# Optimization experiments

Hardware: AMD Instinct MI355X
Metric: run time of the kernel (lower is better)

The kernel has to match this reference:

```python
import jax, jax.numpy as jnp
import numpy as np

NSAMPLES = [64, 32, 16, 8, 4]
TEMPERATURE = 1.0


def square_distance(src, dst):
    # src [B,N,C], dst [B,M,C] -> [B,N,M]
    d = -2.0 * jnp.einsum('bnc,bmc->bnm', src, dst)
    d = d + jnp.sum(src ** 2, -1)[:, :, None]
    d = d + jnp.sum(dst ** 2, -1)[:, None, :]
    return d


def knn_point(nsample, xyz, new_xyz):
    # indices of nsample nearest points in xyz for each query in new_xyz
    sqrdists = square_distance(new_xyz, xyz)           # [B,S,N]
    _, idx = jax.lax.top_k(-sqrdists, nsample)         # smallest distances
    return idx                                         # [B,S,nsample]


def index_points(points, idx):
    # points [B,N,C], idx [B,S,K] -> [B,S,K,C]
    B, S, K = idx.shape
    flat = idx.reshape(B, S * K)
    out = jnp.take_along_axis(points, flat[..., None], axis=1)
    return out.reshape(B, S, K, points.shape[-1])


def boundary_loss(labels, coords, feats, num_classes):
    onehot = jax.nn.one_hot(labels, num_classes, dtype=jnp.float32)  # [B,N,C]
    loss = jnp.float32(0.0)
    for i, (coord, feat) in enumerate(zip(coords, feats)):
        if i == 0:
            probability_labels = onehot
        else:
            kneighbors = i * 4
            nb_idx = knn_point(kneighbors, coords[0], coord)          # [B,Ni,k]
            probability_labels = index_points(onehot, nb_idx).mean(-2)  # [B,Ni,C]
        nsample = NSAMPLES[i]
        neighbor_indexs = knn_point(nsample, coord, coord)            # [B,Ni,ns]
        neighbor_labels = index_points(probability_labels, neighbor_indexs)  # [B,Ni,ns,C]
        neighbor_feats = index_points(feat, neighbor_indexs)          # [B,Ni,ns,D]
        center_label = jnp.argmax(probability_labels, -1)[:, :, None]  # [B,Ni,1]
        neighbor_label = jnp.argmax(neighbor_labels, -1)               # [B,Ni,ns]
        mask = (center_label == neighbor_label)                        # [B,Ni,ns] bool
        cnt = jnp.sum(mask.astype(jnp.int32), -1)
        point_mask = (cnt > 0) & (cnt < nsample)                       # [B,Ni]
        any_pm = jnp.any(point_mask)
        pm = point_mask.astype(jnp.float32)[:, :, None]                # [B,Ni,1]
        # pairwise feature distances to the nsample neighbors
        diff = feat[:, :, None, :] - neighbor_feats                    # [B,Ni,ns,D]
        dist = jnp.sqrt(jnp.sum(diff ** 2, -1) + 1e-6)                 # [B,Ni,ns]
        dist = -dist
        dist = dist - jnp.max(dist, -1, keepdims=True)
        dist = dist / TEMPERATURE
        exp = jnp.exp(dist)
        pos = jnp.sum(exp * mask.astype(jnp.float32) * pm)
        neg = jnp.sum(exp * pm)
        pos = jnp.where(any_pm, pos, 1.0)
        neg = jnp.where(any_pm, neg, 1.0)
        term = -jnp.log(pos / (neg + 1e-6))
        loss = loss + jnp.where(any_pm, term, 0.0)
    return loss


def setup_inputs() -> dict:
    key = jax.random.key(0)
    ks = jax.random.split(key, 12)
    B, N = 2, 4096
    sizes = [N, N // 4, N // 16, N // 64, N // 256]
    inp = {}
    inp['labels'] = jax.random.randint(ks[0], (B, N), 0, 21)
    for i, s in enumerate(sizes):
        inp[f'coord{i}'] = jax.random.normal(ks[1 + i], (B, s, 3), dtype=jnp.float32)
        inp[f'feat{i}'] = jax.random.normal(ks[6 + i], (B, s, 32), dtype=jnp.float32)
    inp['num_classes'] = 21
    return inp


def reference(labels, coord0, coord1, coord2, coord3, coord4,
              feat0, feat1, feat2, feat3, feat4, num_classes):
    coords = [coord0, coord1, coord2, coord3, coord4]
    feats = [feat0, feat1, feat2, feat3, feat4]
    return boundary_loss(labels, coords, feats, num_classes)
```

## Files before the change

kernel.cpp:

```cpp
#include <hip/hip_runtime.h>
#include <math.h>

#define WAVE 64
#define NC 21

__device__ __forceinline__ unsigned f32_ord(float f) {
    unsigned u = __float_as_uint(f);
    return (u & 0x80000000u) ? ~u : (u | 0x80000000u);
}

__device__ __forceinline__ unsigned wave_min_u32(unsigned v) {
#pragma unroll
    for (int off = 32; off >= 1; off >>= 1) {
        unsigned o = (unsigned)__shfl_xor((int)v, off, WAVE);
        v = (o < v) ? o : v;
    }
    return v;
}

__device__ __forceinline__ float wave_max_f32(float v) {
#pragma unroll
    for (int off = 32; off >= 1; off >>= 1)
        v = fmaxf(v, __shfl_xor(v, off, WAVE));
    return v;
}

__device__ __forceinline__ float wave_sum_f32(float v) {
#pragma unroll
    for (int off = 32; off >= 1; off >>= 1)
        v += __shfl_xor(v, off, WAVE);
    return v;
}

struct SelShm {
    int hist[4][256];
    int sel[64];
    int swave[4];
    int scnt;
};

__device__ __forceinline__ void radix_scan_step(SelShm& shm, int lane,
                                                int& need, unsigned& Vhi) {
    int i0 = 4 * lane;
    int b0 = shm.hist[0][i0]   + shm.hist[1][i0]   + shm.hist[2][i0]   + shm.hist[3][i0];
    int b1 = shm.hist[0][i0+1] + shm.hist[1][i0+1] + shm.hist[2][i0+1] + shm.hist[3][i0+1];
    int b2 = shm.hist[0][i0+2] + shm.hist[1][i0+2] + shm.hist[2][i0+2] + shm.hist[3][i0+2];
    int b3 = shm.hist[0][i0+3] + shm.hist[1][i0+3] + shm.hist[2][i0+3] + shm.hist[3][i0+3];
    int lsum = b0 + b1 + b2 + b3;
    int c = lsum;
#pragma unroll
    for (int off = 1; off < 64; off <<= 1) {
        int o = __shfl_up(c, off, WAVE);
        c += (lane >= off) ? o : 0;
    }
    unsigned long long mball = __ballot(c >= need);
    int Ls = __ffsll((unsigned long long)mball) - 1;
    int cL = __shfl(c, Ls, WAVE);
    int lsumL = __shfl(lsum, Ls, WAVE);
    int B0 = __shfl(b0, Ls, WAVE);
    int B1 = __shfl(b1, Ls, WAVE);
    int B2 = __shfl(b2, Ls, WAVE);
    int e = cL - lsumL;
    int T;
    if (e + B0 >= need)                { T = 4 * Ls + 0; }
    else if (e + B0 + B1 >= need)      { T = 4 * Ls + 1; e += B0; }
    else if (e + B0 + B1 + B2 >= need) { T = 4 * Ls + 2; e += B0 + B1; }
    else                               { T = 4 * Ls + 3; e += B0 + B1 + B2; }
    need -= e;
    Vhi = (Vhi << 8) | (unsigned)T;
}

template <int NI, int NS>
__device__ __forceinline__ void block_select_topNS(
    const float* __restrict__ rp,
    float qx, float qy, float qz, float nq,
    SelShm& shm, int tid)
{
    constexpr int NPL = (NI + 255) / 256;
    constexpr bool FULL = (NPL * 256 == NI);
    const int lane = tid & 63;
    const int wid = tid >> 6;
    const unsigned long long lmask = (1ull << lane) - 1ull;

    unsigned ok[NPL];
#pragma unroll
    for (int j = 0; j < NPL; ++j) {
        int g = j * 256 + tid;
        unsigned o = 0xFFFFFFFFu;
        if (FULL || g < NI) {
            float rx = rp[3*g], ry = rp[3*g+1], rz = rp[3*g+2];
            float nr = rx*rx + ry*ry + rz*rz;
            float dot = qx*rx + qy*ry + qz*rz;
            o = f32_ord(-2.0f*dot + nq + nr);
        }
        ok[j] = o;
    }

    int* hf = &shm.hist[0][0];
#pragma unroll
    for (int i = 0; i < 4; ++i) hf[i * 256 + tid] = 0;
    if (tid == 0) shm.scnt = 0;
    __syncthreads();

    int need = NS;
    unsigned Vhi = 0;

#pragma unroll
    for (int j = 0; j < NPL; ++j)
        atomicAdd(&shm.hist[wid][ok[j] >> 24], 1);
    __syncthreads();
    radix_scan_step(shm, lane, need, Vhi);
    __syncthreads();
#pragma unroll
    for (int i = 0; i < 4; ++i) hf[i * 256 + tid] = 0;
    __syncthreads();

#pragma unroll
    for (int pass = 1; pass < 4; ++pass) {
        const int shift = 24 - 8 * pass;
#pragma unroll
        for (int j = 0; j < NPL; ++j) {
            if ((ok[j] >> (shift + 8)) == Vhi)
                atomicAdd(&shm.hist[wid][(ok[j] >> shift) & 255], 1);
        }
        __syncthreads();
        radix_scan_step(shm, lane, need, Vhi);
        __syncthreads();
        if (pass < 3) {
#pragma unroll
            for (int i = 0; i < 4; ++i) hf[i * 256 + tid] = 0;
            __syncthreads();
        }
    }

    const unsigned V = Vhi;
    const int R = need;
    const int clt = NS - R;

#pragma unroll
    for (int j = 0; j < NPL; ++j) {
        bool s = ok[j] < V;
        unsigned long long mk = __ballot(s);
        int n = __popcll(mk);
        if (n) {
            int wb = 0;
            if (lane == 0) wb = atomicAdd(&shm.scnt, n);
            wb = __shfl(wb, 0, WAVE);
            if (s) shm.sel[wb + __popcll(mk & lmask)] = j * 256 + tid;
        }
    }

    unsigned consumed = 0u;
    for (int r = 0; r < R; ++r) {
        int bj = -1;
#pragma unroll
        for (int j = NPL - 1; j >= 0; --j)
            if (ok[j] == V && !((consumed >> j) & 1u)) bj = j;
        unsigned g = (bj >= 0) ? (unsigned)(bj * 256 + tid) : 0xFFFFFFFFu;
        unsigned mg = wave_min_u32(g);
        if (lane == 0) shm.swave[wid] = (int)mg;
        __syncthreads();
        unsigned t0 = (unsigned)shm.swave[0], t1 = (unsigned)shm.swave[1];
        unsigned t2 = (unsigned)shm.swave[2], t3 = (unsigned)shm.swave[3];
        unsigned ta = (t0 < t1) ? t0 : t1;
        unsigned tb = (t2 < t3) ? t2 : t3;
        unsigned t = (ta < tb) ? ta : tb;
        if (bj >= 0 && g == t) consumed |= (1u << bj);
        if (tid == 0) shm.sel[clt + r] = (int)t;
        __syncthreads();
    }
}

template <int NQ, int K>
__device__ __forceinline__ void knn_level(
    const float* __restrict__ qc, const float* __restrict__ rc,
    const int* __restrict__ rl, int* __restrict__ out,
    int qb, SelShm& shm, int tid)
{
    int b = qb / NQ, qi = qb - b * NQ;
    const float* qp = qc + ((long)b * NQ + qi) * 3;
    float qx = qp[0], qy = qp[1], qz = qp[2];
    float nq = qx*qx + qy*qy + qz*qz;
    block_select_topNS<4096, K>(rc + (long)b * 4096 * 3, qx, qy, qz, nq, shm, tid);
    if ((tid >> 6) == 0) {
        int lane = tid & 63;
        int lb = (lane < K) ? rl[(long)b * 4096 + shm.sel[lane]] : -1;
        int cnt = 0;
#pragma unroll
        for (int k = 0; k < K; ++k) {
            int lk = __shfl(lb, k, WAVE);
            cnt += (lk == lane) ? 1 : 0;
        }
        int key = (lane < NC) ? ((cnt << 8) | (255 - lane)) : 0;
#pragma unroll
        for (int off = 32; off >= 1; off >>= 1) {
            int o = __shfl_xor(key, off, WAVE);
            key = (o > key) ? o : key;
        }
        if (lane == 0) out[(long)b * NQ + qi] = 255 - (key & 255);
    }
}

template <int NI, int NS>
__device__ __forceinline__ void boundary_level(
    const float* __restrict__ coord, const float* __restrict__ feat,
    const int* __restrict__ lbl,
    double* __restrict__ pos, double* __restrict__ neg, int* __restrict__ anyf,
    int qb, SelShm& shm, int tid)
{
    int b = qb / NI, qi = qb - b * NI;
    const float* qp = coord + ((long)b * NI + qi) * 3;
    float qx = qp[0], qy = qp[1], qz = qp[2];
    float nq = qx*qx + qy*qy + qz*qz;
    block_select_topNS<NI, NS>(coord + (long)b * NI * 3, qx, qy, qz, nq, shm, tid);
    if ((tid >> 6) == 0) {
        int lane = tid & 63;
        int center = lbl[(long)b * NI + qi];
        bool m = false;
        float dj = -INFINITY;
        if (lane < NS) {
            int nb = shm.sel[lane];
            m = (lbl[(long)b * NI + nb] == center);
            const float4* fq = (const float4*)(feat + ((long)b * NI + qi) * 32);
            const float4* fn = (const float4*)(feat + ((long)b * NI + nb) * 32);
            float s = 0.f;
#pragma unroll
            for (int d = 0; d < 8; ++d) {
                float4 a = fq[d], c = fn[d];
                float d0 = a.x - c.x, d1 = a.y - c.y;
                float d2 = a.z - c.z, d3 = a.w - c.w;
                s += d0*d0 + d1*d1 + d2*d2 + d3*d3;
            }
            dj = -sqrtf(s + 1e-6f);
        }
        unsigned long long mb = __ballot(m);
        int cnt = __popcll(mb);
        float mxv = wave_max_f32(dj);
        float ej = 0.f, pj = 0.f;
        if (lane < NS) {
            ej = expf(dj - mxv);
            pj = m ? ej : 0.f;
        }
        float se = wave_sum_f32(ej);
        float sp = wave_sum_f32(pj);
        bool pm = (cnt > 0) && (cnt < NS);
        if (pm && lane == 0) {
            atomicAdd(pos, (double)sp);
            atomicAdd(neg, (double)se);
            *anyf = 1;
        }
    }
}

__global__ __launch_bounds__(256) void knn_fused(
    const float* __restrict__ c1, const float* __restrict__ c2,
    const float* __restrict__ c3, const float* __restrict__ c4,
    const float* __restrict__ c0, const int* __restrict__ labels,
    int* __restrict__ lbl1, int* __restrict__ lbl2,
    int* __restrict__ lbl3, int* __restrict__ lbl4,
    double* __restrict__ posA, double* __restrict__ negA,
    int* __restrict__ anyA, int B)
{
    __shared__ SelShm shm;
    int blk = blockIdx.x, tid = threadIdx.x;
    int n1 = B * 1024, n2 = n1 + B * 256, n3 = n2 + B * 64, n4 = n3 + B * 16;
    if (blk < n1)      knn_level<1024, 4>(c1, c0, labels, lbl1, blk,      shm, tid);
    else if (blk < n2) knn_level<256,  8>(c2, c0, labels, lbl2, blk - n1, shm, tid);
    else if (blk < n3) knn_level<64,  12>(c3, c0, labels, lbl3, blk - n2, shm, tid);
    else if (blk < n4) knn_level<16,  16>(c4, c0, labels, lbl4, blk - n3, shm, tid);
    else if (tid < 5) { posA[tid] = 0.0; negA[tid] = 0.0; anyA[tid] = 0; }
}

__global__ __launch_bounds__(256) void boundary_fused(
    const float* __restrict__ c0, const float* __restrict__ c1,
    const float* __restrict__ c2, const float* __restrict__ c3,
    const float* __restrict__ c4,
    const float* __restrict__ f0, const float* __restrict__ f1,
    const float* __restrict__ f2, const float* __restrict__ f3,
    const float* __restrict__ f4,
    const int* __restrict__ labels, const int* __restrict__ lbl1,
    const int* __restrict__ lbl2, const int* __restrict__ lbl3,
    const int* __restrict__ lbl4,
    double* __restrict__ posA, double* __restrict__ negA,
    int* __restrict__ anyA, int B)
{
    __shared__ SelShm shm;
    int blk = blockIdx.x, tid = threadIdx.x;
    int m0 = B * 4096, m1 = m0 + B * 1024, m2 = m1 + B * 256;
    int m3 = m2 + B * 64, m4 = m3 + B * 16;
    if (blk < m0)
        boundary_level<4096, 64>(c0, f0, labels, posA+0, negA+0, anyA+0, blk,      shm, tid);
    else if (blk < m1)
        boundary_level<1024, 32>(c1, f1, lbl1,   posA+1, negA+1, anyA+1, blk - m0, shm, tid);
    else if (blk < m2)
        boundary_level<256,  16>(c2, f2, lbl2,   posA+2, negA+2, anyA+2, blk - m1, shm, tid);
    else if (blk < m3)
        boundary_level<64,    8>(c3, f3, lbl3,   posA+3, negA+3, anyA+3, blk - m2, shm, tid);
    else if (blk < m4)
        boundary_level<16,    4>(c4, f4, lbl4,   posA+4, negA+4, anyA+4, blk - m3, shm, tid);
}

__global__ void finalize_kernel(const double* __restrict__ pos,
                                const double* __restrict__ neg,
                                const int* __restrict__ anyf,
                                float* __restrict__ out) {
    if (threadIdx.x == 0 && blockIdx.x == 0) {
        float loss = 0.f;
        for (int i = 0; i < 5; ++i) {
            if (anyf[i]) {
                float p = (float)pos[i];
                float n = (float)neg[i];
                loss += -logf(p / (n + 1e-6f));
            }
        }
        out[0] = loss;
    }
}

extern "C" void kernel_launch(void* const* d_in, const int* in_sizes, int n_in,
                              void* d_out, int out_size, void* d_ws, size_t ws_size,
                              hipStream_t stream) {
    (void)out_size; (void)ws_size;
    const int* labels = (const int*)d_in[0];
    const float* coord[5];
    const float* feat[5];
    bool interleaved = (n_in >= 3 && in_sizes[2] == 2 * 4096 * 32);
    if (interleaved) {
        for (int i = 0; i < 5; ++i) {
            coord[i] = (const float*)d_in[1 + 2 * i];
            feat[i]  = (const float*)d_in[2 + 2 * i];
        }
    } else {
        for (int i = 0; i < 5; ++i) {
            coord[i] = (const float*)d_in[1 + i];
            feat[i]  = (const float*)d_in[6 + i];
        }
    }
    int B = in_sizes[0] / 4096;

    double* posA = (double*)d_ws;
    double* negA = posA + 5;
    int* anyA = (int*)(negA + 5);
    int* lbl1 = anyA + 8;
    int* lbl2 = lbl1 + B * 1024;
    int* lbl3 = lbl2 + B * 256;
    int* lbl4 = lbl3 + B * 64;

    int knn_grid = B * (1024 + 256 + 64 + 16) + 1;
    hipLaunchKernelGGL(knn_fused, dim3(knn_grid), dim3(256), 0, stream,
                       coord[1], coord[2], coord[3], coord[4],
                       coord[0], labels, lbl1, lbl2, lbl3, lbl4,
                       posA, negA, anyA, B);

    int bnd_grid = B * (4096 + 1024 + 256 + 64 + 16);
    hipLaunchKernelGGL(boundary_fused, dim3(bnd_grid), dim3(256), 0, stream,
                       coord[0], coord[1], coord[2], coord[3], coord[4],
                       feat[0], feat[1], feat[2], feat[3], feat[4],
                       labels, lbl1, lbl2, lbl3, lbl4,
                       posA, negA, anyA, B);

    hipLaunchKernelGGL(finalize_kernel, dim3(1), dim3(1), 0, stream,
                       posA, negA, anyA, (float*)d_out);
}
```

Measured before the change: 448.8 us.

## Replace block radix-select kNN with per-wave bitonic top-k with threshold skipping

Swaps the per-query 256-thread block radix select (shared-memory histograms, many __syncthreads, serial tie resolution) for one wavefront per query. Each wave keeps a sorted top-64 list in registers via a bitonic sort and, chunk by chunk, merges in new candidates only when some lane beats the current k-th threshold. This drops the shared memory and block barriers and packs four queries per block. The trade-off is that each wave now scans all reference points itself, so cost depends on how often chunks pass the threshold. Ties are broken by index through the packed 64-bit keys.

Result: slower. 614.9 us (+37.0%).

```diff
diff --git a/kernel.cpp b/kernel.cpp
--- a/kernel.cpp
+++ b/kernel.cpp
@@ -9,15 +9,6 @@
     return (u & 0x80000000u) ? ~u : (u | 0x80000000u);
 }
 
-__device__ __forceinline__ unsigned wave_min_u32(unsigned v) {
-#pragma unroll
-    for (int off = 32; off >= 1; off >>= 1) {
-        unsigned o = (unsigned)__shfl_xor((int)v, off, WAVE);
-        v = (o < v) ? o : v;
-    }
-    return v;
-}
-
 __device__ __forceinline__ float wave_max_f32(float v) {
 #pragma unroll
     for (int off = 32; off >= 1; off >>= 1)
@@ -32,173 +23,104 @@
     return v;
 }
 
-struct SelShm {
-    int hist[4][256];
-    int sel[64];
-    int swave[4];
-    int scnt;
-};
-
-__device__ __forceinline__ void radix_scan_step(SelShm& shm, int lane,
-                                                int& need, unsigned& Vhi) {
-    int i0 = 4 * lane;
-    int b0 = shm.hist[0][i0]   + shm.hist[1][i0]   + shm.hist[2][i0]   + shm.hist[3][i0];
-    int b1 = shm.hist[0][i0+1] + shm.hist[1][i0+1] + shm.hist[2][i0+1] + shm.hist[3][i0+1];
-    int b2 = shm.hist[0][i0+2] + shm.hist[1][i0+2] + shm.hist[2][i0+2] + shm.hist[3][i0+2];
-    int b3 = shm.hist[0][i0+3] + shm.hist[1][i0+3] + shm.hist[2][i0+3] + shm.hist[3][i0+3];
-    int lsum = b0 + b1 + b2 + b3;
-    int c = lsum;
-#pragma unroll
-    for (int off = 1; off < 64; off <<= 1) {
-        int o = __shfl_up(c, off, WAVE);
-        c += (lane >= off) ? o : 0;
-    }
-    unsigned long long mball = __ballot(c >= need);
-    int Ls = __ffsll((unsigned long long)mball) - 1;
-    int cL = __shfl(c, Ls, WAVE);
-    int lsumL = __shfl(lsum, Ls, WAVE);
-    int B0 = __shfl(b0, Ls, WAVE);
-    int B1 = __shfl(b1, Ls, WAVE);
-    int B2 = __shfl(b2, Ls, WAVE);
-    int e = cL - lsumL;
-    int T;
-    if (e + B0 >= need)                { T = 4 * Ls + 0; }
-    else if (e + B0 + B1 >= need)      { T = 4 * Ls + 1; e += B0; }
-    else if (e + B0 + B1 + B2 >= need) { T = 4 * Ls + 2; e += B0 + B1; }
-    else                               { T = 4 * Ls + 3; e += B0 + B1 + B2; }
-    need -= e;
-    Vhi = (Vhi << 8) | (unsigned)T;
+__device__ __forceinline__ unsigned long long bitonic_sort64(
+    unsigned long long v, int lane)
+{
+#pragma unroll
+    for (int k = 2; k <= 64; k <<= 1) {
+#pragma unroll
+        for (int j = k >> 1; j > 0; j >>= 1) {
+            unsigned long long o = __shfl_xor(v, j, WAVE);
+            bool take_min = (((lane & j) == 0) == ((lane & k) == 0));
+            unsigned long long mn = (v < o) ? v : o;
+            unsigned long long mx = (v < o) ? o : v;
+            v = take_min ? mn : mx;
+        }
+    }
+    return v;
+}
+
+__device__ __forceinline__ unsigned long long bitonic_merge_keep_low(
+    unsigned long long h, unsigned long long c, int lane)
+{
+    unsigned long long cr = __shfl(c, 63 - lane, WAVE);
+    unsigned long long v = (h < cr) ? h : cr;
+#pragma unroll
+    for (int j = 32; j > 0; j >>= 1) {
+        unsigned long long o = __shfl_xor(v, j, WAVE);
+        bool take_min = ((lane & j) == 0);
+        unsigned long long mn = (v < o) ? v : o;
+        unsigned long long mx = (v < o) ? o : v;
+        v = take_min ? mn : mx;
+    }
+    return v;
 }
 
 template <int NI, int NS>
-__device__ __forceinline__ void block_select_topNS(
+__device__ __forceinline__ unsigned long long wave_topk(
     const float* __restrict__ rp,
-    float qx, float qy, float qz, float nq,
-    SelShm& shm, int tid)
-{
-    constexpr int NPL = (NI + 255) / 256;
-    constexpr bool FULL = (NPL * 256 == NI);
-    const int lane = tid & 63;
-    const int wid = tid >> 6;
-    const unsigned long long lmask = (1ull << lane) - 1ull;
-
-    unsigned ok[NPL];
-#pragma unroll
-    for (int j = 0; j < NPL; ++j) {
-        int g = j * 256 + tid;
-        unsigned o = 0xFFFFFFFFu;
-        if (FULL || g < NI) {
+    float qx, float qy, float qz, float nq, int lane)
+{
+    constexpr int NCH = (NI + 63) / 64;
+
+    unsigned long long h;
+    {
+        unsigned long long p = ~0ull;
+        if (NI >= 64 || lane < NI) {
+            int g = lane;
             float rx = rp[3*g], ry = rp[3*g+1], rz = rp[3*g+2];
             float nr = rx*rx + ry*ry + rz*rz;
             float dot = qx*rx + qy*ry + qz*rz;
-            o = f32_ord(-2.0f*dot + nq + nr);
-        }
-        ok[j] = o;
-    }
-
-    int* hf = &shm.hist[0][0];
-#pragma unroll
-    for (int i = 0; i < 4; ++i) hf[i * 256 + tid] = 0;
-    if (tid == 0) shm.scnt = 0;
-    __syncthreads();
-
-    int need = NS;
-    unsigned Vhi = 0;
-
-#pragma unroll
-    for (int j = 0; j < NPL; ++j)
-        atomicAdd(&shm.hist[wid][ok[j] >> 24], 1);
-    __syncthreads();
-    radix_scan_step(shm, lane, need, Vhi);
-    __syncthreads();
-#pragma unroll
-    for (int i = 0; i < 4; ++i) hf[i * 256 + tid] = 0;
-    __syncthreads();
-
-#pragma unroll
-    for (int pass = 1; pass < 4; ++pass) {
-        const int shift = 24 - 8 * pass;
-#pragma unroll
-        for (int j = 0; j < NPL; ++j) {
-            if ((ok[j] >> (shift + 8)) == Vhi)
-                atomicAdd(&shm.hist[wid][(ok[j] >> shift) & 255], 1);
-        }
-        __syncthreads();
-        radix_scan_step(shm, lane, need, Vhi);
-        __syncthreads();
-        if (pass < 3) {
-#pragma unroll
-            for (int i = 0; i < 4; ++i) hf[i * 256 + tid] = 0;
-            __syncthreads();
-        }
-    }
-
-    const unsigned V = Vhi;
-    const int R = need;
-    const int clt = NS - R;
-
-#pragma unroll
-    for (int j = 0; j < NPL; ++j) {
-        bool s = ok[j] < V;
-        unsigned long long mk = __ballot(s);
-        int n = __popcll(mk);
-        if (n) {
-            int wb = 0;
-            if (lane == 0) wb = atomicAdd(&shm.scnt, n);
-            wb = __shfl(wb, 0, WAVE);
-            if (s) shm.sel[wb + __popcll(mk & lmask)] = j * 256 + tid;
-        }
-    }
-
-    unsigned consumed = 0u;
-    for (int r = 0; r < R; ++r) {
-        int bj = -1;
-#pragma unroll
-        for (int j = NPL - 1; j >= 0; --j)
-            if (ok[j] == V && !((consumed >> j) & 1u)) bj = j;
-        unsigned g = (bj >= 0) ? (unsigned)(bj * 256 + tid) : 0xFFFFFFFFu;
-        unsigned mg = wave_min_u32(g);
-        if (lane == 0) shm.swave[wid] = (int)mg;
-        __syncthreads();
-        unsigned t0 = (unsigned)shm.swave[0], t1 = (unsigned)shm.swave[1];
-        unsigned t2 = (unsigned)shm.swave[2], t3 = (unsigned)shm.swave[3];
-        unsigned ta = (t0 < t1) ? t0 : t1;
-        unsigned tb = (t2 < t3) ? t2 : t3;
-        unsigned t = (ta < tb) ? ta : tb;
-        if (bj >= 0 && g == t) consumed |= (1u << bj);
-        if (tid == 0) shm.sel[clt + r] = (int)t;
-        __syncthreads();
-    }
+            unsigned o = f32_ord(-2.0f*dot + nq + nr);
+            p = ((unsigned long long)o << 32) | (unsigned)g;
+        }
+        h = bitonic_sort64(p, lane);
+    }
+    if (NCH > 1) {
+        unsigned long long tau = __shfl(h, NS - 1, WAVE);
+#pragma unroll 1
+        for (int cch = 1; cch < NCH; ++cch) {
+            int g = cch * 64 + lane;
+            float rx = rp[3*g], ry = rp[3*g+1], rz = rp[3*g+2];
+            float nr = rx*rx + ry*ry + rz*rz;
+            float dot = qx*rx + qy*ry + qz*rz;
+            unsigned o = f32_ord(-2.0f*dot + nq + nr);
+            unsigned long long p = ((unsigned long long)o << 32) | (unsigned)g;
+            if (__ballot(p < tau) == 0ull) continue;
+            unsigned long long cs = bitonic_sort64(p, lane);
+            h = bitonic_merge_keep_low(h, cs, lane);
+            tau = __shfl(h, NS - 1, WAVE);
+        }
+    }
+    return h;
 }
 
 template <int NQ, int K>
 __device__ __forceinline__ void knn_level(
     const float* __restrict__ qc, const float* __restrict__ rc,
-    const int* __restrict__ rl, int* __restrict__ out,
-    int qb, SelShm& shm, int tid)
-{
-    int b = qb / NQ, qi = qb - b * NQ;
+    const int* __restrict__ rl, int* __restrict__ out, int q, int lane)
+{
+    int b = q / NQ, qi = q - b * NQ;
     const float* qp = qc + ((long)b * NQ + qi) * 3;
     float qx = qp[0], qy = qp[1], qz = qp[2];
     float nq = qx*qx + qy*qy + qz*qz;
-    block_select_topNS<4096, K>(rc + (long)b * 4096 * 3, qx, qy, qz, nq, shm, tid);
-    if ((tid >> 6) == 0) {
-        int lane = tid & 63;
-        int lb = (lane < K) ? rl[(long)b * 4096 + shm.sel[lane]] : -1;
-        int cnt = 0;
-#pragma unroll
-        for (int k = 0; k < K; ++k) {
-            int lk = __shfl(lb, k, WAVE);
-            cnt += (lk == lane) ? 1 : 0;
-        }
-        int key = (lane < NC) ? ((cnt << 8) | (255 - lane)) : 0;
-#pragma unroll
-        for (int off = 32; off >= 1; off >>= 1) {
-            int o = __shfl_xor(key, off, WAVE);
-            key = (o > key) ? o : key;
-        }
-        if (lane == 0) out[(long)b * NQ + qi] = 255 - (key & 255);
-    }
+    unsigned long long h =
+        wave_topk<4096, K>(rc + (long)b * 4096 * 3, qx, qy, qz, nq, lane);
+    int nb = (int)(unsigned)h;
+    int lb = (lane < K) ? rl[(long)b * 4096 + nb] : -1;
+    int cnt = 0;
+#pragma unroll
+    for (int k = 0; k < K; ++k) {
+        int lk = __shfl(lb, k, WAVE);
+        cnt += (lk == lane) ? 1 : 0;
+    }
+    int key = (lane < NC) ? ((cnt << 8) | (255 - lane)) : 0;
+#pragma unroll
+    for (int off = 32; off >= 1; off >>= 1) {
+        int o = __shfl_xor(key, off, WAVE);
+        key = (o > key) ? o : key;
+    }
+    if (lane == 0) out[(long)b * NQ + qi] = 255 - (key & 255);
 }
 
 template <int NI, int NS>
@@ -206,49 +128,47 @@
     const float* __restrict__ coord, const float* __restrict__ feat,
     const int* __restrict__ lbl,
     double* __restrict__ pos, double* __restrict__ neg, int* __restrict__ anyf,
-    int qb, SelShm& shm, int tid)
-{
-    int b = qb / NI, qi = qb - b * NI;
+    int q, int lane)
+{
+    int b = q / NI, qi = q - b * NI;
     const float* qp = coord + ((long)b * NI + qi) * 3;
     float qx = qp[0], qy = qp[1], qz = qp[2];
     float nq = qx*qx + qy*qy + qz*qz;
-    block_select_topNS<NI, NS>(coord + (long)b * NI * 3, qx, qy, qz, nq, shm, tid);
-    if ((tid >> 6) == 0) {
-        int lane = tid & 63;
-        int center = lbl[(long)b * NI + qi];
-        bool m = false;
-        float dj = -INFINITY;
-        if (lane < NS) {
-            int nb = shm.sel[lane];
-            m = (lbl[(long)b * NI + nb] == center);
-            const float4* fq = (const float4*)(feat + ((long)b * NI + qi) * 32);
-            const float4* fn = (const float4*)(feat + ((long)b * NI + nb) * 32);
-            float s = 0.f;
-#pragma unroll
-            for (int d = 0; d < 8; ++d) {
-                float4 a = fq[d], c = fn[d];
-                float d0 = a.x - c.x, d1 = a.y - c.y;
-                float d2 = a.z - c.z, d3 = a.w - c.w;
-                s += d0*d0 + d1*d1 + d2*d2 + d3*d3;
-            }
-            dj = -sqrtf(s + 1e-6f);
-        }
-        unsigned long long mb = __ballot(m);
-        int cnt = __popcll(mb);
-        float mxv = wave_max_f32(dj);
-        float ej = 0.f, pj = 0.f;
-        if (lane < NS) {
-            ej = expf(dj - mxv);
-            pj = m ? ej : 0.f;
-        }
-        float se = wave_sum_f32(ej);
-        float sp = wave_sum_f32(pj);
-        bool pm = (cnt > 0) && (cnt < NS);
-        if (pm && lane == 0) {
-            atomicAdd(pos, (double)sp);
-            atomicAdd(neg, (double)se);
-            *anyf = 1;
-        }
+    unsigned long long h =
+        wave_topk<NI, NS>(coord + (long)b * NI * 3, qx, qy, qz, nq, lane);
+    int nb = (int)(unsigned)h;
+    int center = lbl[(long)b * NI + qi];
+    bool m = false;
+    float dj = -INFINITY;
+    if (lane < NS) {
+        m = (lbl[(long)b * NI + nb] == center);
+        const float4* fq = (const float4*)(feat + ((long)b * NI + qi) * 32);
+        const float4* fn = (const float4*)(feat + ((long)b * NI + nb) * 32);
+        float s = 0.f;
+#pragma unroll
+        for (int d = 0; d < 8; ++d) {
+            float4 a = fq[d], c = fn[d];
+            float d0 = a.x - c.x, d1 = a.y - c.y;
+            float d2 = a.z - c.z, d3 = a.w - c.w;
+            s += d0*d0 + d1*d1 + d2*d2 + d3*d3;
+        }
+        dj = -sqrtf(s + 1e-6f);
+    }
+    unsigned long long mb = __ballot(m);
+    int cnt = __popcll(mb);
+    float mxv = wave_max_f32(dj);
+    float ej = 0.f, pj = 0.f;
+    if (lane < NS) {
+        ej = expf(dj - mxv);
+        pj = m ? ej : 0.f;
+    }
+    float se = wave_sum_f32(ej);
+    float sp = wave_sum_f32(pj);
+    bool pm = (cnt > 0) && (cnt < NS);
+    if (pm && lane == 0) {
+        atomicAdd(pos, (double)sp);
+        atomicAdd(neg, (double)se);
+        *anyf = 1;
     }
 }
 
@@ -261,14 +181,16 @@
     double* __restrict__ posA, double* __restrict__ negA,
     int* __restrict__ anyA, int B)
 {
-    __shared__ SelShm shm;
-    int blk = blockIdx.x, tid = threadIdx.x;
+    int q = blockIdx.x * 4 + (threadIdx.x >> 6);
+    int lane = threadIdx.x & 63;
     int n1 = B * 1024, n2 = n1 + B * 256, n3 = n2 + B * 64, n4 = n3 + B * 16;
-    if (blk < n1)      knn_level<1024, 4>(c1, c0, labels, lbl1, blk,      shm, tid);
-    else if (blk < n2) knn_level<256,  8>(c2, c0, labels, lbl2, blk - n1, shm, tid);
-    else if (blk < n3) knn_level<64,  12>(c3, c0, labels, lbl3, blk - n2, shm, tid);
-    else if (blk < n4) knn_level<16,  16>(c4, c0, labels, lbl4, blk - n3, shm, tid);
-    else if (tid < 5) { posA[tid] = 0.0; negA[tid] = 0.0; anyA[tid] = 0; }
+    if (q < n1)      knn_level<1024, 4>(c1, c0, labels, lbl1, q,      lane);
+    else if (q < n2) knn_level<256,  8>(c2, c0, labels, lbl2, q - n1, lane);
+    else if (q < n3) knn_level<64,  12>(c3, c0, labels, lbl3, q - n2, lane);
+    else if (q < n4) knn_level<16,  16>(c4, c0, labels, lbl4, q - n3, lane);
+    else if (threadIdx.x < 5) {
+        posA[threadIdx.x] = 0.0; negA[threadIdx.x] = 0.0; anyA[threadIdx.x] = 0;
+    }
 }
 
 __global__ __launch_bounds__(256) void boundary_fused(
@@ -284,20 +206,20 @@
     double* __restrict__ posA, double* __restrict__ negA,
     int* __restrict__ anyA, int B)
 {
-    __shared__ SelShm shm;
-    int blk = blockIdx.x, tid = threadIdx.x;
+    int q = blockIdx.x * 4 + (threadIdx.x >> 6);
+    int lane = threadIdx.x & 63;
     int m0 = B * 4096, m1 = m0 + B * 1024, m2 = m1 + B * 256;
     int m3 = m2 + B * 64, m4 = m3 + B * 16;
-    if (blk < m0)
-        boundary_level<4096, 64>(c0, f0, labels, posA+0, negA+0, anyA+0, blk,      shm, tid);
-    else if (blk < m1)
-        boundary_level<1024, 32>(c1, f1, lbl1,   posA+1, negA+1, anyA+1, blk - m0, shm, tid);
-    else if (blk < m2)
-        boundary_level<256,  16>(c2, f2, lbl2,   posA+2, negA+2, anyA+2, blk - m1, shm, tid);
-    else if (blk < m3)
-        boundary_level<64,    8>(c3, f3, lbl3,   posA+3, negA+3, anyA+3, blk - m2, shm, tid);
-    else if (blk < m4)
-        boundary_level<16,    4>(c4, f4, lbl4,   posA+4, negA+4, anyA+4, blk - m3, shm, tid);
+    if (q < m0)
+        boundary_level<4096, 64>(c0, f0, labels, posA+0, negA+0, anyA+0, q,      lane);
+    else if (q < m1)
+        boundary_level<1024, 32>(c1, f1, lbl1,   posA+1, negA+1, anyA+1, q - m0, lane);
+    else if (q < m2)
+        boundary_level<256,  16>(c2, f2, lbl2,   posA+2, negA+2, anyA+2, q - m1, lane);
+    else if (q < m3)
+        boundary_level<64,    8>(c3, f3, lbl3,   posA+3, negA+3, anyA+3, q - m2, lane);
+    else if (q < m4)
+        boundary_level<16,    4>(c4, f4, lbl4,   posA+4, negA+4, anyA+4, q - m3, lane);
 }
 
 __global__ void finalize_kernel(const double* __restrict__ pos,
@@ -346,13 +268,15 @@
     int* lbl3 = lbl2 + B * 256;
     int* lbl4 = lbl3 + B * 64;
 
-    int knn_grid = B * (1024 + 256 + 64 + 16) + 1;
+    int n4 = B * (1024 + 256 + 64 + 16);
+    int knn_grid = (n4 + 3) / 4 + 1;
     hipLaunchKernelGGL(knn_fused, dim3(knn_grid), dim3(256), 0, stream,
                        coord[1], coord[2], coord[3], coord[4],
                        coord[0], labels, lbl1, lbl2, lbl3, lbl4,
                        posA, negA, anyA, B);
 
-    int bnd_grid = B * (4096 + 1024 + 256 + 64 + 16);
+    int m4 = B * (4096 + 1024 + 256 + 64 + 16);
+    int bnd_grid = (m4 + 3) / 4;
     hipLaunchKernelGGL(boundary_fused, dim3(bnd_grid), dim3(256), 0, stream,
                        coord[0], coord[1], coord[2], coord[3], coord[4],
                        feat[0], feat[1], feat[2], feat[3], feat[4],
```
